# Kernel tuning notes

Hardware: AMD Instinct MI355X
Metric: run time of the kernel (lower is better)

The kernel has to match this reference:

```python
import jax, jax.numpy as jnp
import numpy as np

H = 256
B, S, N = 16, 64, 100


def setup_inputs() -> dict:
    key = jax.random.key(0)
    ks = jax.random.split(key, 12)
    def p(k, shape):
        return jax.random.normal(k, shape, dtype=jnp.float32) * 0.02
    z = lambda *s: jnp.zeros(s, jnp.float32)
    return {
        'x': jax.random.normal(ks[0], (B, S, N, H), dtype=jnp.float32),
        'W_ih0': p(ks[1], (4 * H, H)), 'W_hh0': p(ks[2], (4 * H, H)),
        'b_ih0': z(4 * H), 'b_hh0': z(4 * H),
        'W_ih1': p(ks[3], (4 * H, H)), 'W_hh1': p(ks[4], (4 * H, H)),
        'b_ih1': z(4 * H), 'b_hh1': z(4 * H),
        'ln_g': jnp.ones((H,), jnp.float32), 'ln_b': z(H),
        'cen_w1': p(ks[5], (H // 2, H)), 'cen_b1': z(H // 2),
        'cen_w2': p(ks[6], (4, H // 2)), 'cen_b2': z(4),
        'svd_w1': p(ks[7], (H // 2, H)), 'svd_b1': z(H // 2),
        'svd_w2': p(ks[8], (2, H // 2)), 'svd_b2': z(2),
        'lsvd_w1': p(ks[9], (H, H)), 'lsvd_b1': z(H),
        'lsvd_w2': p(ks[10], (16, H)), 'lsvd_b2': z(16),
        'steps': 10,
    }


def reference(x, W_ih0, W_hh0, b_ih0, b_hh0, W_ih1, W_hh1, b_ih1, b_hh1,
              ln_g, ln_b, cen_w1, cen_b1, cen_w2, cen_b2,
              svd_w1, svd_b1, svd_w2, svd_b2,
              lsvd_w1, lsvd_b1, lsvd_w2, lsvd_b2, steps):
    # Dropout layers are identity (eval mode). Per-node Python loop in the
    # original is vectorized by folding nodes into the batch dim (independent
    # LSTM chains share weights and zero-initialized hidden state).
    Bx, Sx, Nx, Hx = x.shape
    BN = Bx * Nx
    xb = x.transpose(0, 2, 1, 3).reshape(BN, Sx, Hx)  # [BN, S, H]

    def cell(xin, h, c, Wih, Whh, bih, bhh):
        g = xin @ Wih.T + bih + h @ Whh.T + bhh
        i, f, gg, o = jnp.split(g, 4, axis=-1)  # torch gate order i,f,g,o
        c = jax.nn.sigmoid(f) * c + jax.nn.sigmoid(i) * jnp.tanh(gg)
        h = jax.nn.sigmoid(o) * jnp.tanh(c)
        return h, c

    def ln(v):
        m = v.mean(-1, keepdims=True)
        var = ((v - m) ** 2).mean(-1, keepdims=True)
        return (v - m) / jnp.sqrt(var + 1e-5) * ln_g + ln_b

    def heads(h):
        cen = jnp.maximum(h @ cen_w1.T + cen_b1, 0.0) @ cen_w2.T + cen_b2
        svd = jnp.maximum(h @ svd_w1.T + svd_b1, 0.0) @ svd_w2.T + svd_b2
        lsvd = jnp.maximum(h @ lsvd_w1.T + lsvd_b1, 0.0) @ lsvd_w2.T + lsvd_b2
        return jnp.concatenate([cen, svd, lsvd], axis=-1)  # [BN, 22]

    zeros = jnp.zeros((BN, Hx), x.dtype)

    def enc_step(carry, xt):
        h0, c0, h1, c1 = carry
        h0, c0 = cell(xt, h0, c0, W_ih0, W_hh0, b_ih0, b_hh0)
        h1, c1 = cell(h0, h1, c1, W_ih1, W_hh1, b_ih1, b_hh1)
        return (h0, c0, h1, c1), None

    (h0, c0, h1, c1), _ = jax.lax.scan(enc_step, (zeros, zeros, zeros, zeros),
                                       xb.transpose(1, 0, 2))
    h_t = ln(h1)  # layernorm of last encoder output

    def dec_step(carry, _):
        ht, h0, c0, h1, c1 = carry
        pred = heads(ht)
        h0n, c0n = cell(ht, h0, c0, W_ih0, W_hh0, b_ih0, b_hh0)
        h1n, c1n = cell(h0n, h1, c1, W_ih1, W_hh1, b_ih1, b_hh1)
        return (ln(h1n), h0n, c0n, h1n, c1n), pred

    _, preds = jax.lax.scan(dec_step, (h_t, h0, c0, h1, c1), None, length=steps)
    # preds: [steps, BN, 22] -> [B, steps, N, 22]
    return preds.reshape(steps, Bx, Nx, 22).transpose(1, 0, 2, 3)
```

## Files before the change

### kernel.cpp

```cpp
#include <hip/hip_runtime.h>
#include <hip/hip_bf16.h>
#include <stdint.h>


#define H 256
#define SS 64
#define NN 100
#define BNROWS 1600
#define KD 512
#define STEPS 10

typedef __bf16 bf16_t;
typedef __attribute__((ext_vector_type(8))) __bf16 bf16x8;
typedef __attribute__((ext_vector_type(4))) __bf16 bf16x4;
typedef __attribute__((ext_vector_type(4))) float f32x4;
typedef __attribute__((ext_vector_type(4))) unsigned uint4v;

__device__ __forceinline__ float sigm(float x) { return 1.0f / (1.0f + __expf(-x)); }
__device__ __forceinline__ float tanh_c(float x) {
    x = fminf(fmaxf(x, -15.0f), 15.0f);
    float e = __expf(2.0f * x);
    return (e - 1.0f) / (e + 1.0f);
}

__device__ __forceinline__ unsigned ld_sys(const unsigned* p) {
    return __hip_atomic_load(p, __ATOMIC_RELAXED, __HIP_MEMORY_SCOPE_SYSTEM);
}
__device__ __forceinline__ void st_sys(unsigned* p, unsigned v) {
    __hip_atomic_store(p, v, __ATOMIC_RELAXED, __HIP_MEMORY_SCOPE_SYSTEM);
}
__device__ __forceinline__ uint4v ld16_sys(const void* p) {
    uint4v v;
    asm volatile("global_load_dwordx4 %0, %1, off sc0 sc1"
                 : "=v"(v) : "v"(p) : "memory");
    return v;
}
__device__ __forceinline__ unsigned pack_bf16(float a, float b) {
    bf16_t xa = (bf16_t)a, xb = (bf16_t)b;
    unsigned short ua, ub;
    __builtin_memcpy(&ua, &xa, 2);
    __builtin_memcpy(&ub, &xb, 2);
    return (unsigned)ua | ((unsigned)ub << 16);
}
__device__ __forceinline__ float bf16lo(unsigned u) {
    unsigned v = u << 16; float f; __builtin_memcpy(&f, &v, 4); return f;
}
__device__ __forceinline__ float bf16hi(unsigned u) {
    unsigned v = u & 0xffff0000u; float f; __builtin_memcpy(&f, &v, 4); return f;
}
__device__ __forceinline__ float u2f(unsigned u) {
    float f; __builtin_memcpy(&f, &u, 4); return f;
}
__device__ __forceinline__ unsigned f2u(float f) {
    unsigned u; __builtin_memcpy(&u, &f, 4); return u;
}

__global__ __launch_bounds__(256)
void prep_kernel(const float* __restrict__ Wih0, const float* __restrict__ Whh0,
                 const float* __restrict__ bih0, const float* __restrict__ bhh0,
                 const float* __restrict__ Wih1, const float* __restrict__ Whh1,
                 const float* __restrict__ bih1, const float* __restrict__ bhh1,
                 const float* __restrict__ cw1, const float* __restrict__ sw1,
                 const float* __restrict__ lw1,
                 const float* __restrict__ cb1, const float* __restrict__ sb1,
                 const float* __restrict__ lb1,
                 bf16_t* __restrict__ W0c, bf16_t* __restrict__ W1c,
                 bf16_t* __restrict__ Wh1, float* __restrict__ bias0,
                 float* __restrict__ bias1, float* __restrict__ biash)
{
    int idx = blockIdx.x * 256 + threadIdx.x;
    if (idx < 524288) {
        int nr = idx >> 9, k = idx & 511;
        int j = nr >> 2, gi = nr & 3;
        int go = gi * 256 + j;
        float v = (k < 256) ? Wih0[go * 256 + k] : Whh0[go * 256 + (k - 256)];
        W0c[idx] = (bf16_t)v;
        return;
    }
    idx -= 524288;
    if (idx < 524288) {
        int nr = idx >> 9, k = idx & 511;
        int j = nr >> 2, gi = nr & 3;
        int go = gi * 256 + j;
        float v = (k < 256) ? Wih1[go * 256 + k] : Whh1[go * 256 + (k - 256)];
        W1c[idx] = (bf16_t)v;
        return;
    }
    idx -= 524288;
    if (idx < 131072) {
        int r = idx >> 8, k = idx & 255;
        float v = (r < 128) ? cw1[r * 256 + k]
                            : (r < 256 ? sw1[(r - 128) * 256 + k]
                                       : lw1[(r - 256) * 256 + k]);
        Wh1[idx] = (bf16_t)v;
        return;
    }
    idx -= 131072;
    if (idx < 1024) {
        int j = idx >> 2, gi = idx & 3, go = gi * 256 + j;
        bias0[idx] = bih0[go] + bhh0[go];
        return;
    }
    idx -= 1024;
    if (idx < 1024) {
        int j = idx >> 2, gi = idx & 3, go = gi * 256 + j;
        bias1[idx] = bih1[go] + bhh1[go];
        return;
    }
    idx -= 1024;
    if (idx < 512) {
        biash[idx] = (idx < 128) ? cb1[idx]
                                 : (idx < 256 ? sb1[idx - 128] : lb1[idx - 256]);
    }
}

__global__ __launch_bounds__(256)
void xconv_kernel(const float* __restrict__ x, bf16_t* __restrict__ xb)
{
    int o = (blockIdx.x * 256 + threadIdx.x) * 4;
    int s = o / 409600;
    int rem = o - s * 409600;
    int m = rem >> 8;
    int h = rem & 255;
    int b = m / 100, n = m - b * 100;
    const float* src = x + (((size_t)(b * 64 + s) * 100 + n) << 8) + h;
    f32x4 v = *(const f32x4*)src;
    bf16x4 ov;
    ov[0] = (bf16_t)v.x; ov[1] = (bf16_t)v.y; ov[2] = (bf16_t)v.z; ov[3] = (bf16_t)v.w;
    *(bf16x4*)(xb + o) = ov;
}

struct PA {
    const bf16_t* xb;
    const bf16_t* W0c; const bf16_t* W1c; const bf16_t* Wh1;
    const float* bias0; const float* bias1; const float* biash;
    const float* lng; const float* lnb;
    const float* cw2; const float* cb2;
    const float* sw2; const float* sb2;
    const float* lw2; const float* lb2;
    bf16_t* h0a; bf16_t* h0b; bf16_t* h1a; bf16_t* h1b;
    bf16_t* ht; float* hid;
    unsigned* cnt;
    float* out;
};

__global__ __launch_bounds__(256, 2)
void persistent_kernel(PA p)
{
    __shared__ uint4v smem[4160];

    const int tid  = threadIdx.x;
    const int w    = tid >> 6;
    const int lane = tid & 63;
    const int quad = lane >> 4;
    const int l16  = lane & 15;
    const bool isL0 = (blockIdx.x < 200);
    const int cb   = isL0 ? (int)blockIdx.x : (int)blockIdx.x - 200;
    const int mt   = cb >> 3;
    const int nt   = cb & 7;
    const int bg   = nt + (isL0 ? 0 : 8);
    const int mbase = mt * 64;
    const int nbase = nt * 128 + w * 32;
    const int hcb   = nbase >> 2;
    float* Gw = (float*)smem + w * 2304;

    const int trow  = tid >> 6;
    const int tcol8 = (tid & 63) * 8;
    const bool firsthalf = (tcol8 < 256);
    const int coladj = firsthalf ? tcol8 : tcol8 - 256;
    const size_t stagebyte = ((size_t)(mbase + trow) * 256 + coladj) * 2;

    unsigned* cntg = p.cnt + mt * 64;
    unsigned rnd = 0;
    auto bar = [&]() {
        ++rnd;
        asm volatile("s_waitcnt vmcnt(0) lgkmcnt(0)" ::: "memory");
        __syncthreads();
        if (tid == 0) {
            __hip_atomic_fetch_add(cntg, 1u, __ATOMIC_RELAXED,
                                   __HIP_MEMORY_SCOPE_SYSTEM);
            while (__hip_atomic_load(cntg, __ATOMIC_RELAXED,
                                     __HIP_MEMORY_SCOPE_SYSTEM) < 16u * rnd) { }
        }
        __syncthreads();
    };

    bf16_t* h0buf[2] = { p.h0a, p.h0b };
    bf16_t* h1buf[2] = { p.h1a, p.h1b };

    float bv[2];
    {
        const float* br = isL0 ? p.bias0 : p.bias1;
        #pragma unroll
        for (int nf = 0; nf < 2; ++nf) bv[nf] = br[nbase + nf * 16 + l16];
    }
    const int hb1 = nt * 64 + w * 16;
    const float bh = p.biash[hb1 + l16];
    float lgv[4], lbv[4];
    #pragma unroll
    for (int j = 0; j < 4; ++j) { lgv[j] = p.lng[lane * 4 + j]; lbv[j] = p.lnb[lane * 4 + j]; }

    const bf16_t* Wc = isL0 ? p.W0c : p.W1c;
    bf16x8 Breg[2][16];
    #pragma unroll
    for (int nf = 0; nf < 2; ++nf)
        #pragma unroll
        for (int kf = 0; kf < 16; ++kf)
            Breg[nf][kf] = *(const bf16x8*)(Wc + (size_t)(nbase + nf * 16 + l16) * KD
                                            + kf * 32 + quad * 8);

    float creg[8];
    #pragma unroll
    for (int e = 0; e < 8; ++e) creg[e] = 0.0f;

    auto cellw = [&](const bf16_t* sA, const bf16_t* sB, bf16_t* hd) {
        {
            const char* sp = (const char*)(firsthalf ? sA : sB) + stagebyte;
            uint4v c[8];
            #pragma unroll
            for (int i = 0; i < 8; ++i) c[i] = ld16_sys(sp + (size_t)i * 2048);
            asm volatile("s_waitcnt vmcnt(0)" ::: "memory");
            #pragma unroll
            for (int i = 0; i < 8; ++i)
                *(uint4v*)((char*)smem + (size_t)(trow + i * 4) * 1040 + tcol8 * 2) = c[i];
            #pragma unroll
            for (int i = 0; i < 8; ++i) c[i] = ld16_sys(sp + (size_t)(i + 8) * 2048);
            asm volatile("s_waitcnt vmcnt(0)" ::: "memory");
            #pragma unroll
            for (int i = 0; i < 8; ++i)
                *(uint4v*)((char*)smem + (size_t)(trow + (i + 8) * 4) * 1040 + tcol8 * 2) = c[i];
        }
        __syncthreads();

        f32x4 zero4 = {0.f, 0.f, 0.f, 0.f};
        f32x4 acc[4][2];
        #pragma unroll
        for (int mf = 0; mf < 4; ++mf)
            #pragma unroll
            for (int nf = 0; nf < 2; ++nf) acc[mf][nf] = zero4;

        #pragma unroll
        for (int kf = 0; kf < 16; ++kf) {
            bf16x8 af[4];
            #pragma unroll
            for (int mf = 0; mf < 4; ++mf)
                af[mf] = *(const bf16x8*)((char*)smem
                            + (size_t)(mf * 16 + l16) * 1040 + kf * 64 + quad * 16);
            #pragma unroll
            for (int mf = 0; mf < 4; ++mf)
                #pragma unroll
                for (int nf = 0; nf < 2; ++nf)
                    acc[mf][nf] = __builtin_amdgcn_mfma_f32_16x16x32_bf16(
                        af[mf], Breg[nf][kf], acc[mf][nf], 0, 0, 0);
        }
        __syncthreads();

        #pragma unroll
        for (int mf = 0; mf < 4; ++mf)
            #pragma unroll
            for (int nf = 0; nf < 2; ++nf)
                #pragma unroll
                for (int r = 0; r < 4; ++r)
                    Gw[(mf * 16 + quad * 4 + r) * 36 + nf * 16 + l16] =
                        acc[mf][nf][r] + bv[nf];
        asm volatile("s_waitcnt lgkmcnt(0)" ::: "memory");

        #pragma unroll
        for (int e = 0; e < 4; ++e) {
            int ml  = e * 16 + (lane >> 2);
            int jl2 = (lane & 3) * 2;
            f32x4 ga = *(const f32x4*)(Gw + ml * 36 + jl2 * 4);
            f32x4 gb = *(const f32x4*)(Gw + ml * 36 + jl2 * 4 + 4);
            float cn0 = sigm(ga.y) * creg[e * 2] + sigm(ga.x) * tanh_c(ga.z);
            float cn1 = sigm(gb.y) * creg[e * 2 + 1] + sigm(gb.x) * tanh_c(gb.z);
            creg[e * 2]     = cn0;
            creg[e * 2 + 1] = cn1;
            float hn0 = sigm(ga.w) * tanh_c(cn0);
            float hn1 = sigm(gb.w) * tanh_c(cn1);
            st_sys((unsigned*)(hd + (size_t)(mbase + ml) * H + hcb + jl2),
                   pack_bf16(hn0, hn1));
        }
    };

    auto heads1w = [&]() {
        {
            const int hrow0 = tid >> 5;
            const int hcol8 = (tid & 31) * 8;
            const char* sp = (const char*)p.ht
                + ((size_t)(mbase + hrow0) * 256 + hcol8) * 2;
            uint4v c[8];
            #pragma unroll
            for (int i = 0; i < 8; ++i) c[i] = ld16_sys(sp + (size_t)i * 4096);
            asm volatile("s_waitcnt vmcnt(0)" ::: "memory");
            #pragma unroll
            for (int i = 0; i < 8; ++i)
                *(uint4v*)((char*)smem + (size_t)(hrow0 + i * 8) * 1040 + hcol8 * 2) = c[i];
        }
        __syncthreads();

        f32x4 zero4 = {0.f, 0.f, 0.f, 0.f};
        f32x4 ha[4] = {zero4, zero4, zero4, zero4};
        #pragma unroll
        for (int kf = 0; kf < 8; ++kf) {
            bf16x8 bb = *(const bf16x8*)(p.Wh1 + (size_t)(hb1 + l16) * H
                                         + kf * 32 + quad * 8);
            #pragma unroll
            for (int mf = 0; mf < 4; ++mf) {
                bf16x8 af = *(const bf16x8*)((char*)smem
                            + (size_t)(mf * 16 + l16) * 1040 + kf * 64 + quad * 16);
                ha[mf] = __builtin_amdgcn_mfma_f32_16x16x32_bf16(af, bb, ha[mf], 0, 0, 0);
            }
        }
        #pragma unroll
        for (int mf = 0; mf < 4; ++mf)
            #pragma unroll
            for (int r = 0; r < 4; ++r) {
                int mg = mbase + mf * 16 + quad * 4 + r;
                int ng = hb1 + l16;
                float v = fmaxf(ha[mf][r] + bh, 0.0f);
                st_sys((unsigned*)(p.hid + (size_t)mg * 512 + ng), f2u(v));
            }
    };

    auto heads2w = [&](int s) {
        int idx = nt * 256 + tid;
        if (idx >= 64 * 22) return;
        int lr = idx / 22;
        int o  = idx - lr * 22;
        int m  = mbase + lr;
        const unsigned* hrow = (const unsigned*)(p.hid + (size_t)m * 512);
        const float* wp; float bias; int k0, len;
        if (o < 4)      { wp = p.cw2 + o * 128;       bias = p.cb2[o];     k0 = 0;   len = 128; }
        else if (o < 6) { wp = p.sw2 + (o - 4) * 128; bias = p.sb2[o - 4]; k0 = 128; len = 128; }
        else            { wp = p.lw2 + (o - 6) * 256; bias = p.lb2[o - 6]; k0 = 256; len = 256; }
        float acc = bias;
        for (int k = 0; k < len; k += 4) {
            f32x4 wv = *(const f32x4*)(wp + k);
            acc += u2f(ld_sys(hrow + k0 + k))     * wv.x;
            acc += u2f(ld_sys(hrow + k0 + k + 1)) * wv.y;
            acc += u2f(ld_sys(hrow + k0 + k + 2)) * wv.z;
            acc += u2f(ld_sys(hrow + k0 + k + 3)) * wv.w;
        }
        int b = m / NN, n = m - b * NN;
        p.out[(((size_t)b * STEPS + s) * NN + n) * 22 + o] = acc;
    };

    auto lnw = [&](const bf16_t* src) {
        int sample = mbase + bg * 4 + w;
        const unsigned* rp = (const unsigned*)(src + (size_t)sample * H) + lane * 2;
        unsigned u0 = ld_sys(rp), u1 = ld_sys(rp + 1);
        float v[4] = { bf16lo(u0), bf16hi(u0), bf16lo(u1), bf16hi(u1) };
        float sm = v[0] + v[1] + v[2] + v[3];
        #pragma unroll
        for (int off = 32; off > 0; off >>= 1) sm += __shfl_xor(sm, off);
        float mean = sm * (1.0f / H);
        float q = 0.f;
        #pragma unroll
        for (int j = 0; j < 4; ++j) { float d = v[j] - mean; q += d * d; }
        #pragma unroll
        for (int off = 32; off > 0; off >>= 1) q += __shfl_xor(q, off);
        float rstd = rsqrtf(q * (1.0f / H) + 1e-5f);
        float o0 = (v[0] - mean) * rstd * lgv[0] + lbv[0];
        float o1 = (v[1] - mean) * rstd * lgv[1] + lbv[1];
        float o2 = (v[2] - mean) * rstd * lgv[2] + lbv[2];
        float o3 = (v[3] - mean) * rstd * lgv[3] + lbv[3];
        unsigned* wp2 = (unsigned*)(p.ht + (size_t)sample * H) + lane * 2;
        st_sys(wp2,     pack_bf16(o0, o1));
        st_sys(wp2 + 1, pack_bf16(o2, o3));
    };

    #pragma unroll 1
    for (int r = 0; r < 65; ++r) {
        if (isL0) {
            if (r < 64)
                cellw(p.xb + (size_t)r * 409600, h0buf[(r + 1) & 1], h0buf[r & 1]);
        } else {
            if (r >= 1)
                cellw(h0buf[(r + 1) & 1], h1buf[r & 1], h1buf[(r + 1) & 1]);
        }
        bar();
    }
    lnw(h1buf[1]);
    bar();

    #pragma unroll 1
    for (int s = 0; s < STEPS; ++s) {
        if (isL0) cellw(p.ht, h0buf[(s + 1) & 1], h0buf[s & 1]);
        else      heads1w();
        bar();
        if (!isL0) cellw(h0buf[s & 1], h1buf[(s + 1) & 1], h1buf[s & 1]);
        else       heads2w(s);
        bar();
        if (s < STEPS - 1) { lnw(h1buf[s & 1]); bar(); }
    }
}

__global__ __launch_bounds__(256)
void cell_kernel(const float* __restrict__ xsrc, int t,
                 const bf16_t* __restrict__ a1,
                 const bf16_t* __restrict__ a2,
                 const bf16_t* __restrict__ Wc,
                 const float* __restrict__ biasr,
                 float* __restrict__ cst,
                 bf16_t* __restrict__ hout)
{
    __shared__ char smem_raw[18432];
    bf16_t* As = (bf16_t*)smem_raw;
    bf16_t* Bs = (bf16_t*)(smem_raw + 9216);
    float*  Gsf = (float*)smem_raw;

    const int tid  = threadIdx.x;
    const int mblk = blockIdx.x;
    const int nblk = blockIdx.y;
    const int am = tid >> 2;
    const int kc = (tid & 3) << 4;
    const int gm = mblk * 64 + am;

    const float*  xrow  = nullptr;
    const bf16_t* arow1 = nullptr;
    if (xsrc) {
        int b = gm / NN;
        int n = gm - b * NN;
        xrow = xsrc + (((size_t)b * SS + t) * NN + n) * H;
    } else {
        arow1 = a1 + (size_t)gm * H;
    }
    const bf16_t* arow2 = a2 + (size_t)gm * H;
    const bf16_t* brow  = Wc + (size_t)(nblk * 64 + am) * KD;

    bf16x8 ra0, ra1, rb0, rb1;
    auto loadA = [&](int ko) {
        int k = ko + kc;
        if (xsrc) {
            if (k < 256) {
                const f32x4* pq = (const f32x4*)(xrow + k);
                f32x4 f0 = pq[0], f1 = pq[1], f2 = pq[2], f3 = pq[3];
                bf16x8 v0, v1;
                v0[0]=(bf16_t)f0.x; v0[1]=(bf16_t)f0.y; v0[2]=(bf16_t)f0.z; v0[3]=(bf16_t)f0.w;
                v0[4]=(bf16_t)f1.x; v0[5]=(bf16_t)f1.y; v0[6]=(bf16_t)f1.z; v0[7]=(bf16_t)f1.w;
                v1[0]=(bf16_t)f2.x; v1[1]=(bf16_t)f2.y; v1[2]=(bf16_t)f2.z; v1[3]=(bf16_t)f2.w;
                v1[4]=(bf16_t)f3.x; v1[5]=(bf16_t)f3.y; v1[6]=(bf16_t)f3.z; v1[7]=(bf16_t)f3.w;
                ra0 = v0; ra1 = v1;
            } else {
                const bf16x8* pq = (const bf16x8*)(arow2 + (k - 256));
                ra0 = pq[0]; ra1 = pq[1];
            }
        } else {
            const bf16x8* pq = (k < 256) ? (const bf16x8*)(arow1 + k)
                                         : (const bf16x8*)(arow2 + (k - 256));
            ra0 = pq[0]; ra1 = pq[1];
        }
    };
    auto loadB = [&](int ko) {
        const bf16x8* pq = (const bf16x8*)(brow + ko + kc);
        rb0 = pq[0]; rb1 = pq[1];
    };
    loadA(0); loadB(0);

    const int w    = tid >> 6;
    const int lane = tid & 63;
    const int wm   = w & 1, wn = w >> 1;
    const int quad = lane >> 4, l16 = lane & 15;

    f32x4 zero4 = {0.f, 0.f, 0.f, 0.f};
    f32x4 acc[2][2] = {{zero4, zero4}, {zero4, zero4}};

    for (int kk = 0; kk < 8; ++kk) {
        __syncthreads();
        *(bf16x8*)(As + am * 72 + kc)     = ra0;
        *(bf16x8*)(As + am * 72 + kc + 8) = ra1;
        *(bf16x8*)(Bs + am * 72 + kc)     = rb0;
        *(bf16x8*)(Bs + am * 72 + kc + 8) = rb1;
        __syncthreads();
        if (kk < 7) { loadA((kk + 1) * 64); loadB((kk + 1) * 64); }
        #pragma unroll
        for (int ks = 0; ks < 2; ++ks) {
            bf16x8 af[2], bb[2];
            #pragma unroll
            for (int mi = 0; mi < 2; ++mi)
                af[mi] = *(const bf16x8*)(As + (wm * 32 + mi * 16 + l16) * 72 + ks * 32 + quad * 8);
            #pragma unroll
            for (int ni = 0; ni < 2; ++ni)
                bb[ni] = *(const bf16x8*)(Bs + (wn * 32 + ni * 16 + l16) * 72 + ks * 32 + quad * 8);
            #pragma unroll
            for (int mi = 0; mi < 2; ++mi)
                #pragma unroll
                for (int ni = 0; ni < 2; ++ni)
                    acc[mi][ni] = __builtin_amdgcn_mfma_f32_16x16x32_bf16(
                        af[mi], bb[ni], acc[mi][ni], 0, 0, 0);
        }
    }

    __syncthreads();
    float bvv[2];
    #pragma unroll
    for (int ni = 0; ni < 2; ++ni)
        bvv[ni] = biasr[nblk * 64 + wn * 32 + ni * 16 + l16];

    #pragma unroll
    for (int mi = 0; mi < 2; ++mi)
        #pragma unroll
        for (int ni = 0; ni < 2; ++ni)
            #pragma unroll
            for (int r = 0; r < 4; ++r) {
                int ml = wm * 32 + mi * 16 + quad * 4 + r;
                int nl = wn * 32 + ni * 16 + l16;
                Gsf[ml * 68 + nl] = acc[mi][ni][r] + bvv[ni];
            }
    __syncthreads();

    #pragma unroll
    for (int e = 0; e < 4; ++e) {
        int id = tid + 256 * e;
        int ml = id >> 4;
        int jl = id & 15;
        f32x4 g4 = *(const f32x4*)(Gsf + ml * 68 + jl * 4);
        int gmm = mblk * 64 + ml;
        int jg  = nblk * 16 + jl;
        float co = cst[(size_t)gmm * H + jg];
        float iv = sigm(g4.x);
        float fv = sigm(g4.y);
        float gv = tanh_c(g4.z);
        float ov = sigm(g4.w);
        float cn = fv * co + iv * gv;
        float hn = ov * tanh_c(cn);
        cst[(size_t)gmm * H + jg]  = cn;
        hout[(size_t)gmm * H + jg] = (bf16_t)hn;
    }
}

__global__ __launch_bounds__(256)
void heads1_kernel(const bf16_t* __restrict__ a1,
                   const bf16_t* __restrict__ Wh,
                   const float* __restrict__ biash,
                   bf16_t* __restrict__ hid)
{
    __shared__ char smem_raw[18432];
    bf16_t* As = (bf16_t*)smem_raw;
    bf16_t* Bs = (bf16_t*)(smem_raw + 9216);

    const int tid  = threadIdx.x;
    const int mblk = blockIdx.x;
    const int nblk = blockIdx.y;
    const int am = tid >> 2;
    const int kc = (tid & 3) << 4;
    const int gm = mblk * 64 + am;
    const bf16_t* arow = a1 + (size_t)gm * H;
    const bf16_t* brow = Wh + (size_t)(nblk * 64 + am) * H;

    bf16x8 ra0, ra1, rb0, rb1;
    auto load = [&](int ko) {
        const bf16x8* pa = (const bf16x8*)(arow + ko + kc);
        ra0 = pa[0]; ra1 = pa[1];
        const bf16x8* pb = (const bf16x8*)(brow + ko + kc);
        rb0 = pb[0]; rb1 = pb[1];
    };
    load(0);

    const int w    = tid >> 6;
    const int lane = tid & 63;
    const int wm   = w & 1, wn = w >> 1;
    const int quad = lane >> 4, l16 = lane & 15;

    f32x4 zero4 = {0.f, 0.f, 0.f, 0.f};
    f32x4 acc[2][2] = {{zero4, zero4}, {zero4, zero4}};

    for (int kk = 0; kk < 4; ++kk) {
        __syncthreads();
        *(bf16x8*)(As + am * 72 + kc)     = ra0;
        *(bf16x8*)(As + am * 72 + kc + 8) = ra1;
        *(bf16x8*)(Bs + am * 72 + kc)     = rb0;
        *(bf16x8*)(Bs + am * 72 + kc + 8) = rb1;
        __syncthreads();
        if (kk < 3) load((kk + 1) * 64);
        #pragma unroll
        for (int ks = 0; ks < 2; ++ks) {
            bf16x8 af[2], bb[2];
            #pragma unroll
            for (int mi = 0; mi < 2; ++mi)
                af[mi] = *(const bf16x8*)(As + (wm * 32 + mi * 16 + l16) * 72 + ks * 32 + quad * 8);
            #pragma unroll
            for (int ni = 0; ni < 2; ++ni)
                bb[ni] = *(const bf16x8*)(Bs + (wn * 32 + ni * 16 + l16) * 72 + ks * 32 + quad * 8);
            #pragma unroll
            for (int mi = 0; mi < 2; ++mi)
                #pragma unroll
                for (int ni = 0; ni < 2; ++ni)
                    acc[mi][ni] = __builtin_amdgcn_mfma_f32_16x16x32_bf16(
                        af[mi], bb[ni], acc[mi][ni], 0, 0, 0);
        }
    }

    #pragma unroll
    for (int mi = 0; mi < 2; ++mi)
        #pragma unroll
        for (int ni = 0; ni < 2; ++ni)
            #pragma unroll
            for (int r = 0; r < 4; ++r) {
                int mg = mblk * 64 + wm * 32 + mi * 16 + quad * 4 + r;
                int ng = nblk * 64 + wn * 32 + ni * 16 + l16;
                float v = acc[mi][ni][r] + biash[ng];
                hid[(size_t)mg * 512 + ng] = (bf16_t)fmaxf(v, 0.0f);
            }
}

__global__ __launch_bounds__(256)
void heads2_kernel(const bf16_t* __restrict__ hid,
                   const float* __restrict__ cw2, const float* __restrict__ cb2,
                   const float* __restrict__ sw2, const float* __restrict__ sb2,
                   const float* __restrict__ lw2, const float* __restrict__ lb2,
                   float* __restrict__ out, int s)
{
    int idx = blockIdx.x * 256 + threadIdx.x;
    if (idx >= BNROWS * 22) return;
    int m = idx / 22;
    int o = idx - m * 22;
    const bf16_t* hrow = hid + (size_t)m * 512;
    const float* wp; float bias; int k0, len;
    if (o < 4)      { wp = cw2 + o * 128;       bias = cb2[o];     k0 = 0;   len = 128; }
    else if (o < 6) { wp = sw2 + (o - 4) * 128; bias = sb2[o - 4]; k0 = 128; len = 128; }
    else            { wp = lw2 + (o - 6) * 256; bias = lb2[o - 6]; k0 = 256; len = 256; }
    float acc = bias;
    for (int k = 0; k < len; k += 4) {
        f32x4 wv = *(const f32x4*)(wp + k);
        acc += (float)hrow[k0 + k]     * wv.x;
        acc += (float)hrow[k0 + k + 1] * wv.y;
        acc += (float)hrow[k0 + k + 2] * wv.z;
        acc += (float)hrow[k0 + k + 3] * wv.w;
    }
    int b = m / NN, n = m - b * NN;
    out[(((size_t)b * STEPS + s) * NN + n) * 22 + o] = acc;
}

__global__ __launch_bounds__(256)
void ln_kernel(const bf16_t* __restrict__ hin,
               const float* __restrict__ gam, const float* __restrict__ bet,
               bf16_t* __restrict__ hto)
{
    int w = threadIdx.x >> 6;
    int lane = threadIdx.x & 63;
    int sample = blockIdx.x * 4 + w;
    const bf16_t* row = hin + (size_t)sample * H;
    float v[4];
    #pragma unroll
    for (int j = 0; j < 4; ++j) v[j] = (float)row[lane * 4 + j];
    float sm = v[0] + v[1] + v[2] + v[3];
    #pragma unroll
    for (int off = 32; off > 0; off >>= 1) sm += __shfl_xor(sm, off);
    float mean = sm * (1.0f / H);
    float q = 0.f;
    #pragma unroll
    for (int j = 0; j < 4; ++j) { float d = v[j] - mean; q += d * d; }
    #pragma unroll
    for (int off = 32; off > 0; off >>= 1) q += __shfl_xor(q, off);
    float rstd = rsqrtf(q * (1.0f / H) + 1e-5f);
    #pragma unroll
    for (int j = 0; j < 4; ++j) {
        int idx = lane * 4 + j;
        float o = (v[j] - mean) * rstd * gam[idx] + bet[idx];
        hto[(size_t)sample * H + idx] = (bf16_t)o;
    }
}

extern "C" void kernel_launch(void* const* d_in, const int* in_sizes, int n_in,
                              void* d_out, int out_size, void* d_ws, size_t ws_size,
                              hipStream_t stream)
{
    const float* x    = (const float*)d_in[0];
    const float* Wih0 = (const float*)d_in[1];
    const float* Whh0 = (const float*)d_in[2];
    const float* bih0 = (const float*)d_in[3];
    const float* bhh0 = (const float*)d_in[4];
    const float* Wih1 = (const float*)d_in[5];
    const float* Whh1 = (const float*)d_in[6];
    const float* bih1 = (const float*)d_in[7];
    const float* bhh1 = (const float*)d_in[8];
    const float* lng  = (const float*)d_in[9];
    const float* lnb  = (const float*)d_in[10];
    const float* cw1  = (const float*)d_in[11];
    const float* cb1  = (const float*)d_in[12];
    const float* cw2  = (const float*)d_in[13];
    const float* cb2  = (const float*)d_in[14];
    const float* sw1  = (const float*)d_in[15];
    const float* sb1  = (const float*)d_in[16];
    const float* sw2  = (const float*)d_in[17];
    const float* sb2  = (const float*)d_in[18];
    const float* lw1  = (const float*)d_in[19];
    const float* lb1  = (const float*)d_in[20];
    const float* lw2  = (const float*)d_in[21];
    const float* lb2  = (const float*)d_in[22];
    float* out = (float*)d_out;

    char* ws = (char*)d_ws;
    if (ws_size < 62200000) return;

    bf16_t* W0c   = (bf16_t*)(ws);
    bf16_t* W1c   = (bf16_t*)(ws + 1048576);
    bf16_t* Wh1w  = (bf16_t*)(ws + 2097152);
    float*  bias0 = (float*)(ws + 2359296);
    float*  bias1 = (float*)(ws + 2363392);
    float*  biash = (float*)(ws + 2367488);
    char* st = ws + 2369536;
    bf16_t* h0a = (bf16_t*)st;
    bf16_t* h0b = (bf16_t*)(st + 819200);
    bf16_t* h1a = (bf16_t*)(st + 1638400);
    bf16_t* h1b = (bf16_t*)(st + 2457600);
    bf16_t* ht  = (bf16_t*)(st + 3276800);
    float*  hid = (float*)(st + 4096000);
    unsigned* cnt = (unsigned*)(st + 7372800);
    bf16_t* xb  = (bf16_t*)(st + 7379200);
    float* c0 = (float*)(st + 7379200);
    float* c1 = (float*)(st + 9017600);

    hipMemsetAsync(st, 0, 3276800, stream);
    hipMemsetAsync(cnt, 0, 6400, stream);

    prep_kernel<<<4615, 256, 0, stream>>>(Wih0, Whh0, bih0, bhh0,
                                          Wih1, Whh1, bih1, bhh1,
                                          cw1, sw1, lw1, cb1, sb1, lb1,
                                          W0c, W1c, Wh1w, bias0, bias1, biash);
    xconv_kernel<<<25600, 256, 0, stream>>>(x, xb);

    PA pa;
    pa.xb = xb; pa.W0c = W0c; pa.W1c = W1c; pa.Wh1 = Wh1w;
    pa.bias0 = bias0; pa.bias1 = bias1; pa.biash = biash;
    pa.lng = lng; pa.lnb = lnb;
    pa.cw2 = cw2; pa.cb2 = cb2; pa.sw2 = sw2; pa.sb2 = sb2;
    pa.lw2 = lw2; pa.lb2 = lb2;
    pa.h0a = h0a; pa.h0b = h0b; pa.h1a = h1a; pa.h1b = h1b;
    pa.ht = ht; pa.hid = hid; pa.cnt = cnt; pa.out = out;

    void* kargs[] = { &pa };
    hipError_t err = hipLaunchCooperativeKernel((void*)persistent_kernel,
                                                dim3(400), dim3(256),
                                                kargs, 0, stream);
    if (err == hipSuccess) return;

    hipMemsetAsync(c0, 0, 1638400, stream);
    hipMemsetAsync(c1, 0, 1638400, stream);
    bf16_t* hidb = (bf16_t*)hid;
    bf16_t* h0buf[2] = { h0a, h0b };
    bf16_t* h1buf[2] = { h1a, h1b };
    dim3 cg2(25, 16);
    int cur = 0;
    for (int t = 0; t < SS; ++t) {
        cell_kernel<<<cg2, 256, 0, stream>>>(x, t, nullptr, h0buf[cur], W0c, bias0,
                                             c0, h0buf[cur ^ 1]);
        cell_kernel<<<cg2, 256, 0, stream>>>(nullptr, 0, h0buf[cur ^ 1], h1buf[cur],
                                             W1c, bias1, c1, h1buf[cur ^ 1]);
        cur ^= 1;
    }
    ln_kernel<<<400, 256, 0, stream>>>(h1buf[cur], lng, lnb, ht);
    for (int s = 0; s < STEPS; ++s) {
        heads1_kernel<<<dim3(25, 8), 256, 0, stream>>>(ht, Wh1w, biash, hidb);
        heads2_kernel<<<138, 256, 0, stream>>>(hidb, cw2, cb2, sw2, sb2, lw2, lb2,
                                               out, s);
        cell_kernel<<<cg2, 256, 0, stream>>>(nullptr, 0, ht, h0buf[cur], W0c, bias0,
                                             c0, h0buf[cur ^ 1]);
        cell_kernel<<<cg2, 256, 0, stream>>>(nullptr, 0, h0buf[cur ^ 1], h1buf[cur],
                                             W1c, bias1, c1, h1buf[cur ^ 1]);
        cur ^= 1;
        ln_kernel<<<400, 256, 0, stream>>>(h1buf[cur], lng, lnb, ht);
    }
}
```

Before: 1.257 ms.

## Use per-block flag barrier, transposed MFMA cell epilogue, and bf16 head hidden

Replaces the atomic-counter group barrier with per-block flag stores that are polled using vector loads, which removes contended atomics. The MFMA operands are swapped so each lane holds all four gates of a hidden unit in registers. The LSTM cell update then runs directly from the accumulators, skipping the fp32 LDS gate round-trip and one __syncthreads. Outputs go through a small LDS transpose into coalesced 16-byte system-scope stores. The heads hidden buffer changes from fp32 to bf16 and is read with vector loads, which cuts traffic but adds rounding error to the heads.

```diff
diff --git a/kernel.cpp b/kernel.cpp
--- a/kernel.cpp
+++ b/kernel.cpp
@@ -22,19 +22,6 @@
     float e = __expf(2.0f * x);
     return (e - 1.0f) / (e + 1.0f);
 }
-
-__device__ __forceinline__ unsigned ld_sys(const unsigned* p) {
-    return __hip_atomic_load(p, __ATOMIC_RELAXED, __HIP_MEMORY_SCOPE_SYSTEM);
-}
-__device__ __forceinline__ void st_sys(unsigned* p, unsigned v) {
-    __hip_atomic_store(p, v, __ATOMIC_RELAXED, __HIP_MEMORY_SCOPE_SYSTEM);
-}
-__device__ __forceinline__ uint4v ld16_sys(const void* p) {
-    uint4v v;
-    asm volatile("global_load_dwordx4 %0, %1, off sc0 sc1"
-                 : "=v"(v) : "v"(p) : "memory");
-    return v;
-}
 __device__ __forceinline__ unsigned pack_bf16(float a, float b) {
     bf16_t xa = (bf16_t)a, xb = (bf16_t)b;
     unsigned short ua, ub;
@@ -48,12 +35,22 @@
 __device__ __forceinline__ float bf16hi(unsigned u) {
     unsigned v = u & 0xffff0000u; float f; __builtin_memcpy(&f, &v, 4); return f;
 }
-__device__ __forceinline__ float u2f(unsigned u) {
-    float f; __builtin_memcpy(&f, &u, 4); return f;
-}
-__device__ __forceinline__ unsigned f2u(float f) {
-    unsigned u; __builtin_memcpy(&u, &f, 4); return u;
-}
+__device__ __forceinline__ uint4v ld16_sys(const void* p) {
+    uint4v v;
+    asm volatile("global_load_dwordx4 %0, %1, off sc0 sc1"
+                 : "=v"(v) : "v"(p) : "memory");
+    return v;
+}
+__device__ __forceinline__ void st16_sys(void* p, uint4v v) {
+    asm volatile("global_store_dwordx4 %0, %1, off sc0 sc1" :: "v"(p), "v"(v) : "memory");
+}
+__device__ __forceinline__ void st4_sys(void* p, unsigned v) {
+    asm volatile("global_store_dword %0, %1, off sc0 sc1" :: "v"(p), "v"(v) : "memory");
+}
+__device__ __forceinline__ unsigned ld4_sys(const unsigned* p) {
+    return __hip_atomic_load(p, __ATOMIC_RELAXED, __HIP_MEMORY_SCOPE_SYSTEM);
+}
+#define VM_DRAIN() asm volatile("s_waitcnt vmcnt(0)" ::: "memory")
 
 __global__ __launch_bounds__(256)
 void prep_kernel(const float* __restrict__ Wih0, const float* __restrict__ Whh0,
@@ -139,15 +136,16 @@
     const float* sw2; const float* sb2;
     const float* lw2; const float* lb2;
     bf16_t* h0a; bf16_t* h0b; bf16_t* h1a; bf16_t* h1b;
-    bf16_t* ht; float* hid;
-    unsigned* cnt;
+    bf16_t* ht; bf16_t* hid;
+    unsigned* flags;
     float* out;
 };
 
 __global__ __launch_bounds__(256, 2)
 void persistent_kernel(PA p)
 {
-    __shared__ uint4v smem[4160];
+    __shared__ char stageLDS[66560];
+    __shared__ char tbuf[8192];
 
     const int tid  = threadIdx.x;
     const int w    = tid >> 6;
@@ -156,31 +154,33 @@
     const int l16  = lane & 15;
     const bool isL0 = (blockIdx.x < 200);
     const int cb   = isL0 ? (int)blockIdx.x : (int)blockIdx.x - 200;
-    const int mt   = cb >> 3;
+    const int grp  = cb >> 3;
     const int nt   = cb & 7;
     const int bg   = nt + (isL0 ? 0 : 8);
-    const int mbase = mt * 64;
+    const int mbase = grp * 64;
     const int nbase = nt * 128 + w * 32;
-    const int hcb   = nbase >> 2;
-    float* Gw = (float*)smem + w * 2304;
-
-    const int trow  = tid >> 6;
-    const int tcol8 = (tid & 63) * 8;
-    const bool firsthalf = (tcol8 < 256);
-    const int coladj = firsthalf ? tcol8 : tcol8 - 256;
-    const size_t stagebyte = ((size_t)(mbase + trow) * 256 + coladj) * 2;
-
-    unsigned* cntg = p.cnt + mt * 64;
+    const int hb    = nt * 64 + w * 16;
+
+    unsigned* fl = p.flags + grp * 64;
     unsigned rnd = 0;
     auto bar = [&]() {
         ++rnd;
-        asm volatile("s_waitcnt vmcnt(0) lgkmcnt(0)" ::: "memory");
+        VM_DRAIN();
         __syncthreads();
         if (tid == 0) {
-            __hip_atomic_fetch_add(cntg, 1u, __ATOMIC_RELAXED,
-                                   __HIP_MEMORY_SCOPE_SYSTEM);
-            while (__hip_atomic_load(cntg, __ATOMIC_RELAXED,
-                                     __HIP_MEMORY_SCOPE_SYSTEM) < 16u * rnd) { }
+            st4_sys(fl + bg, rnd);
+            for (;;) {
+                uint4v a = ld16_sys(fl);
+                uint4v b = ld16_sys(fl + 4);
+                uint4v c = ld16_sys(fl + 8);
+                uint4v d = ld16_sys(fl + 12);
+                VM_DRAIN();
+                unsigned m = min(min(min(a[0], a[1]), min(a[2], a[3])),
+                                 min(min(b[0], b[1]), min(b[2], b[3])));
+                m = min(m, min(min(min(c[0], c[1]), min(c[2], c[3])),
+                               min(min(d[0], d[1]), min(d[2], d[3]))));
+                if (m >= rnd) break;
+            }
         }
         __syncthreads();
     };
@@ -188,138 +188,122 @@
     bf16_t* h0buf[2] = { p.h0a, p.h0b };
     bf16_t* h1buf[2] = { p.h1a, p.h1b };
 
-    float bv[2];
-    {
-        const float* br = isL0 ? p.bias0 : p.bias1;
-        #pragma unroll
-        for (int nf = 0; nf < 2; ++nf) bv[nf] = br[nbase + nf * 16 + l16];
-    }
-    const int hb1 = nt * 64 + w * 16;
-    const float bh = p.biash[hb1 + l16];
-    float lgv[4], lbv[4];
-    #pragma unroll
-    for (int j = 0; j < 4; ++j) { lgv[j] = p.lng[lane * 4 + j]; lbv[j] = p.lnb[lane * 4 + j]; }
-
     const bf16_t* Wc = isL0 ? p.W0c : p.W1c;
     bf16x8 Breg[2][16];
     #pragma unroll
-    for (int nf = 0; nf < 2; ++nf)
+    for (int gt = 0; gt < 2; ++gt)
         #pragma unroll
         for (int kf = 0; kf < 16; ++kf)
-            Breg[nf][kf] = *(const bf16x8*)(Wc + (size_t)(nbase + nf * 16 + l16) * KD
+            Breg[gt][kf] = *(const bf16x8*)(Wc + (size_t)(nbase + gt * 16 + l16) * KD
                                             + kf * 32 + quad * 8);
+    const float* br = isL0 ? p.bias0 : p.bias1;
+    f32x4 bvq[2];
+    bvq[0] = *(const f32x4*)(br + nbase + quad * 4);
+    bvq[1] = *(const f32x4*)(br + nbase + 16 + quad * 4);
+    f32x4 bhq = *(const f32x4*)(p.biash + hb + quad * 4);
+    float lgv[4], lbv[4];
+    #pragma unroll
+    for (int j = 0; j < 4; ++j) { lgv[j] = p.lng[lane * 4 + j]; lbv[j] = p.lnb[lane * 4 + j]; }
 
     float creg[8];
     #pragma unroll
     for (int e = 0; e < 8; ++e) creg[e] = 0.0f;
 
-    auto cellw = [&](const bf16_t* sA, const bf16_t* sB, bf16_t* hd) {
-        {
-            const char* sp = (const char*)(firsthalf ? sA : sB) + stagebyte;
-            uint4v c[8];
-            #pragma unroll
-            for (int i = 0; i < 8; ++i) c[i] = ld16_sys(sp + (size_t)i * 2048);
-            asm volatile("s_waitcnt vmcnt(0)" ::: "memory");
-            #pragma unroll
-            for (int i = 0; i < 8; ++i)
-                *(uint4v*)((char*)smem + (size_t)(trow + i * 4) * 1040 + tcol8 * 2) = c[i];
-            #pragma unroll
-            for (int i = 0; i < 8; ++i) c[i] = ld16_sys(sp + (size_t)(i + 8) * 2048);
-            asm volatile("s_waitcnt vmcnt(0)" ::: "memory");
-            #pragma unroll
-            for (int i = 0; i < 8; ++i)
-                *(uint4v*)((char*)smem + (size_t)(trow + (i + 8) * 4) * 1040 + tcol8 * 2) = c[i];
-        }
+    auto stage2 = [&](const bf16_t* s1, const bf16_t* s2) {
+        const char* sel = (lane < 32) ? (const char*)s1 : ((const char*)s2 - 512);
+        const char* gp = sel + (size_t)(mbase + w * 16) * 512 + lane * 16;
+        uint4v t[16];
+        #pragma unroll
+        for (int i = 0; i < 16; ++i) t[i] = ld16_sys(gp + (size_t)i * 512);
+        VM_DRAIN();
+        char* lp = stageLDS + (w * 16) * 1040 + lane * 16;
+        #pragma unroll
+        for (int i = 0; i < 16; ++i) *(uint4v*)(lp + i * 1040) = t[i];
         __syncthreads();
-
+    };
+
+    auto cellw = [&](const bf16_t* s1, const bf16_t* s2, bf16_t* hd) {
+        stage2(s1, s2);
         f32x4 zero4 = {0.f, 0.f, 0.f, 0.f};
-        f32x4 acc[4][2];
-        #pragma unroll
-        for (int mf = 0; mf < 4; ++mf)
-            #pragma unroll
-            for (int nf = 0; nf < 2; ++nf) acc[mf][nf] = zero4;
-
+        f32x4 acc[2][4];
+        #pragma unroll
+        for (int gt = 0; gt < 2; ++gt)
+            #pragma unroll
+            for (int mt = 0; mt < 4; ++mt) acc[gt][mt] = zero4;
         #pragma unroll
         for (int kf = 0; kf < 16; ++kf) {
             bf16x8 af[4];
             #pragma unroll
-            for (int mf = 0; mf < 4; ++mf)
-                af[mf] = *(const bf16x8*)((char*)smem
-                            + (size_t)(mf * 16 + l16) * 1040 + kf * 64 + quad * 16);
-            #pragma unroll
-            for (int mf = 0; mf < 4; ++mf)
+            for (int mt = 0; mt < 4; ++mt)
+                af[mt] = *(const bf16x8*)(stageLDS + (size_t)(mt * 16 + l16) * 1040
+                                          + kf * 64 + quad * 16);
+            #pragma unroll
+            for (int gt = 0; gt < 2; ++gt)
                 #pragma unroll
-                for (int nf = 0; nf < 2; ++nf)
-                    acc[mf][nf] = __builtin_amdgcn_mfma_f32_16x16x32_bf16(
-                        af[mf], Breg[nf][kf], acc[mf][nf], 0, 0, 0);
-        }
-        __syncthreads();
-
-        #pragma unroll
-        for (int mf = 0; mf < 4; ++mf)
-            #pragma unroll
-            for (int nf = 0; nf < 2; ++nf)
-                #pragma unroll
-                for (int r = 0; r < 4; ++r)
-                    Gw[(mf * 16 + quad * 4 + r) * 36 + nf * 16 + l16] =
-                        acc[mf][nf][r] + bv[nf];
+                for (int mt = 0; mt < 4; ++mt)
+                    acc[gt][mt] = __builtin_amdgcn_mfma_f32_16x16x32_bf16(
+                        Breg[gt][kf], af[mt], acc[gt][mt], 0, 0, 0);
+        }
+        bf16_t* tb = (bf16_t*)(tbuf + w * 2048);
+        #pragma unroll
+        for (int gt = 0; gt < 2; ++gt)
+            #pragma unroll
+            for (int mt = 0; mt < 4; ++mt) {
+                f32x4 g4 = acc[gt][mt] + bvq[gt];
+                int ci = gt * 4 + mt;
+                float cn = sigm(g4.y) * creg[ci] + sigm(g4.x) * tanh_c(g4.z);
+                creg[ci] = cn;
+                tb[(mt * 16 + l16) * 8 + gt * 4 + quad] = (bf16_t)(sigm(g4.w) * tanh_c(cn));
+            }
         asm volatile("s_waitcnt lgkmcnt(0)" ::: "memory");
-
-        #pragma unroll
-        for (int e = 0; e < 4; ++e) {
-            int ml  = e * 16 + (lane >> 2);
-            int jl2 = (lane & 3) * 2;
-            f32x4 ga = *(const f32x4*)(Gw + ml * 36 + jl2 * 4);
-            f32x4 gb = *(const f32x4*)(Gw + ml * 36 + jl2 * 4 + 4);
-            float cn0 = sigm(ga.y) * creg[e * 2] + sigm(ga.x) * tanh_c(ga.z);
-            float cn1 = sigm(gb.y) * creg[e * 2 + 1] + sigm(gb.x) * tanh_c(gb.z);
-            creg[e * 2]     = cn0;
-            creg[e * 2 + 1] = cn1;
-            float hn0 = sigm(ga.w) * tanh_c(cn0);
-            float hn1 = sigm(gb.w) * tanh_c(cn1);
-            st_sys((unsigned*)(hd + (size_t)(mbase + ml) * H + hcb + jl2),
-                   pack_bf16(hn0, hn1));
-        }
+        bf16x8 hv = *(const bf16x8*)(tb + lane * 8);
+        st16_sys((char*)hd + ((size_t)(mbase + lane) * 256 + nt * 32 + w * 8) * 2,
+                 *(uint4v*)&hv);
     };
 
     auto heads1w = [&]() {
         {
             const int hrow0 = tid >> 5;
             const int hcol8 = (tid & 31) * 8;
-            const char* sp = (const char*)p.ht
+            const char* gp = (const char*)p.ht
                 + ((size_t)(mbase + hrow0) * 256 + hcol8) * 2;
-            uint4v c[8];
-            #pragma unroll
-            for (int i = 0; i < 8; ++i) c[i] = ld16_sys(sp + (size_t)i * 4096);
-            asm volatile("s_waitcnt vmcnt(0)" ::: "memory");
+            uint4v t[8];
+            #pragma unroll
+            for (int i = 0; i < 8; ++i) t[i] = ld16_sys(gp + (size_t)i * 4096);
+            VM_DRAIN();
             #pragma unroll
             for (int i = 0; i < 8; ++i)
-                *(uint4v*)((char*)smem + (size_t)(hrow0 + i * 8) * 1040 + hcol8 * 2) = c[i];
+                *(uint4v*)(stageLDS + (size_t)(hrow0 + i * 8) * 1040 + hcol8 * 2) = t[i];
         }
         __syncthreads();
-
         f32x4 zero4 = {0.f, 0.f, 0.f, 0.f};
         f32x4 ha[4] = {zero4, zero4, zero4, zero4};
         #pragma unroll
         for (int kf = 0; kf < 8; ++kf) {
-            bf16x8 bb = *(const bf16x8*)(p.Wh1 + (size_t)(hb1 + l16) * H
+            bf16x8 bb = *(const bf16x8*)(p.Wh1 + (size_t)(hb + l16) * 256
                                          + kf * 32 + quad * 8);
             #pragma unroll
-            for (int mf = 0; mf < 4; ++mf) {
-                bf16x8 af = *(const bf16x8*)((char*)smem
-                            + (size_t)(mf * 16 + l16) * 1040 + kf * 64 + quad * 16);
-                ha[mf] = __builtin_amdgcn_mfma_f32_16x16x32_bf16(af, bb, ha[mf], 0, 0, 0);
+            for (int mt = 0; mt < 4; ++mt) {
+                bf16x8 af = *(const bf16x8*)(stageLDS + (size_t)(mt * 16 + l16) * 1040
+                                             + kf * 64 + quad * 16);
+                ha[mt] = __builtin_amdgcn_mfma_f32_16x16x32_bf16(bb, af, ha[mt], 0, 0, 0);
             }
         }
-        #pragma unroll
-        for (int mf = 0; mf < 4; ++mf)
-            #pragma unroll
-            for (int r = 0; r < 4; ++r) {
-                int mg = mbase + mf * 16 + quad * 4 + r;
-                int ng = hb1 + l16;
-                float v = fmaxf(ha[mf][r] + bh, 0.0f);
-                st_sys((unsigned*)(p.hid + (size_t)mg * 512 + ng), f2u(v));
-            }
+        bf16_t* tb = (bf16_t*)(tbuf + w * 2048);
+        #pragma unroll
+        for (int mt = 0; mt < 4; ++mt) {
+            f32x4 v = ha[mt] + bhq;
+            bf16x4 pk;
+            #pragma unroll
+            for (int r = 0; r < 4; ++r) pk[r] = (bf16_t)fmaxf(v[r], 0.0f);
+            *(bf16x4*)(tb + (mt * 16 + l16) * 16 + quad * 4) = pk;
+        }
+        asm volatile("s_waitcnt lgkmcnt(0)" ::: "memory");
+        bf16x8 v0 = *(const bf16x8*)(tb + lane * 16);
+        bf16x8 v1 = *(const bf16x8*)(tb + lane * 16 + 8);
+        char* dst = (char*)p.hid + ((size_t)(mbase + lane) * 512 + hb) * 2;
+        st16_sys(dst, *(uint4v*)&v0);
+        st16_sys(dst + 16, *(uint4v*)&v1);
     };
 
     auto heads2w = [&](int s) {
@@ -328,18 +312,29 @@
         int lr = idx / 22;
         int o  = idx - lr * 22;
         int m  = mbase + lr;
-        const unsigned* hrow = (const unsigned*)(p.hid + (size_t)m * 512);
+        const char* hrow = (const char*)(p.hid + (size_t)m * 512);
         const float* wp; float bias; int k0, len;
         if (o < 4)      { wp = p.cw2 + o * 128;       bias = p.cb2[o];     k0 = 0;   len = 128; }
         else if (o < 6) { wp = p.sw2 + (o - 4) * 128; bias = p.sb2[o - 4]; k0 = 128; len = 128; }
         else            { wp = p.lw2 + (o - 6) * 256; bias = p.lb2[o - 6]; k0 = 256; len = 256; }
         float acc = bias;
-        for (int k = 0; k < len; k += 4) {
-            f32x4 wv = *(const f32x4*)(wp + k);
-            acc += u2f(ld_sys(hrow + k0 + k))     * wv.x;
-            acc += u2f(ld_sys(hrow + k0 + k + 1)) * wv.y;
-            acc += u2f(ld_sys(hrow + k0 + k + 2)) * wv.z;
-            acc += u2f(ld_sys(hrow + k0 + k + 3)) * wv.w;
+        for (int kb = 0; kb < len; kb += 64) {
+            uint4v hv[8];
+            #pragma unroll
+            for (int i = 0; i < 8; ++i)
+                hv[i] = ld16_sys(hrow + (size_t)(k0 + kb + i * 8) * 2);
+            VM_DRAIN();
+            #pragma unroll
+            for (int i = 0; i < 8; ++i) {
+                bf16x8 h8 = *(bf16x8*)&hv[i];
+                const float* wpp = wp + kb + i * 8;
+                f32x4 w0 = *(const f32x4*)wpp;
+                f32x4 w1 = *(const f32x4*)(wpp + 4);
+                acc += (float)h8[0] * w0.x + (float)h8[1] * w0.y
+                     + (float)h8[2] * w0.z + (float)h8[3] * w0.w
+                     + (float)h8[4] * w1.x + (float)h8[5] * w1.y
+                     + (float)h8[6] * w1.z + (float)h8[7] * w1.w;
+            }
         }
         int b = m / NN, n = m - b * NN;
         p.out[(((size_t)b * STEPS + s) * NN + n) * 22 + o] = acc;
@@ -348,7 +343,7 @@
     auto lnw = [&](const bf16_t* src) {
         int sample = mbase + bg * 4 + w;
         const unsigned* rp = (const unsigned*)(src + (size_t)sample * H) + lane * 2;
-        unsigned u0 = ld_sys(rp), u1 = ld_sys(rp + 1);
+        unsigned u0 = ld4_sys(rp), u1 = ld4_sys(rp + 1);
         float v[4] = { bf16lo(u0), bf16hi(u0), bf16lo(u1), bf16hi(u1) };
         float sm = v[0] + v[1] + v[2] + v[3];
         #pragma unroll
@@ -365,8 +360,8 @@
         float o2 = (v[2] - mean) * rstd * lgv[2] + lbv[2];
         float o3 = (v[3] - mean) * rstd * lgv[3] + lbv[3];
         unsigned* wp2 = (unsigned*)(p.ht + (size_t)sample * H) + lane * 2;
-        st_sys(wp2,     pack_bf16(o0, o1));
-        st_sys(wp2 + 1, pack_bf16(o2, o3));
+        st4_sys(wp2,     pack_bf16(o0, o1));
+        st4_sys(wp2 + 1, pack_bf16(o2, o3));
     };
 
     #pragma unroll 1
@@ -434,12 +429,12 @@
         if (xsrc) {
             if (k < 256) {
                 const f32x4* pq = (const f32x4*)(xrow + k);
-                f32x4 f0 = pq[0], f1 = pq[1], f2 = pq[2], f3 = pq[3];
+                f32x4 fq0 = pq[0], fq1 = pq[1], fq2 = pq[2], fq3 = pq[3];
                 bf16x8 v0, v1;
-                v0[0]=(bf16_t)f0.x; v0[1]=(bf16_t)f0.y; v0[2]=(bf16_t)f0.z; v0[3]=(bf16_t)f0.w;
-                v0[4]=(bf16_t)f1.x; v0[5]=(bf16_t)f1.y; v0[6]=(bf16_t)f1.z; v0[7]=(bf16_t)f1.w;
-                v1[0]=(bf16_t)f2.x; v1[1]=(bf16_t)f2.y; v1[2]=(bf16_t)f2.z; v1[3]=(bf16_t)f2.w;
-                v1[4]=(bf16_t)f3.x; v1[5]=(bf16_t)f3.y; v1[6]=(bf16_t)f3.z; v1[7]=(bf16_t)f3.w;
+                v0[0]=(bf16_t)fq0.x; v0[1]=(bf16_t)fq0.y; v0[2]=(bf16_t)fq0.z; v0[3]=(bf16_t)fq0.w;
+                v0[4]=(bf16_t)fq1.x; v0[5]=(bf16_t)fq1.y; v0[6]=(bf16_t)fq1.z; v0[7]=(bf16_t)fq1.w;
+                v1[0]=(bf16_t)fq2.x; v1[1]=(bf16_t)fq2.y; v1[2]=(bf16_t)fq2.z; v1[3]=(bf16_t)fq2.w;
+                v1[4]=(bf16_t)fq3.x; v1[5]=(bf16_t)fq3.y; v1[6]=(bf16_t)fq3.z; v1[7]=(bf16_t)fq3.w;
                 ra0 = v0; ra1 = v1;
             } else {
                 const bf16x8* pq = (const bf16x8*)(arow2 + (k - 256));
@@ -518,14 +513,9 @@
         int gmm = mblk * 64 + ml;
         int jg  = nblk * 16 + jl;
         float co = cst[(size_t)gmm * H + jg];
-        float iv = sigm(g4.x);
-        float fv = sigm(g4.y);
-        float gv = tanh_c(g4.z);
-        float ov = sigm(g4.w);
-        float cn = fv * co + iv * gv;
-        float hn = ov * tanh_c(cn);
+        float cn = sigm(g4.y) * co + sigm(g4.x) * tanh_c(g4.z);
         cst[(size_t)gmm * H + jg]  = cn;
-        hout[(size_t)gmm * H + jg] = (bf16_t)hn;
+        hout[(size_t)gmm * H + jg] = (bf16_t)(sigm(g4.w) * tanh_c(cn));
     }
 }
 
@@ -692,7 +682,7 @@
     float* out = (float*)d_out;
 
     char* ws = (char*)d_ws;
-    if (ws_size < 62200000) return;
+    if (ws_size < 65000000) return;
 
     bf16_t* W0c   = (bf16_t*)(ws);
     bf16_t* W1c   = (bf16_t*)(ws + 1048576);
@@ -706,16 +696,16 @@
     bf16_t* h1a = (bf16_t*)(st + 1638400);
     bf16_t* h1b = (bf16_t*)(st + 2457600);
     bf16_t* ht  = (bf16_t*)(st + 3276800);
-    float*  hid = (float*)(st + 4096000);
-    unsigned* cnt = (unsigned*)(st + 7372800);
-    bf16_t* xb  = (bf16_t*)(st + 7379200);
-    float* c0 = (float*)(st + 7379200);
-    float* c1 = (float*)(st + 9017600);
+    bf16_t* hid = (bf16_t*)(st + 4096000);
+    unsigned* flg = (unsigned*)(st + 5734400);
+    bf16_t* xb  = (bf16_t*)(st + 5740800);
+    float* fc0 = (float*)(st + 5740800);
+    float* fc1 = (float*)(st + 7379200);
 
     hipMemsetAsync(st, 0, 3276800, stream);
-    hipMemsetAsync(cnt, 0, 6400, stream);
-
-    prep_kernel<<<4615, 256, 0, stream>>>(Wih0, Whh0, bih0, bhh0,
+    hipMemsetAsync(flg, 0, 6400, stream);
+
+    prep_kernel<<<4618, 256, 0, stream>>>(Wih0, Whh0, bih0, bhh0,
                                           Wih1, Whh1, bih1, bhh1,
                                           cw1, sw1, lw1, cb1, sb1, lb1,
                                           W0c, W1c, Wh1w, bias0, bias1, biash);
@@ -728,7 +718,7 @@
     pa.cw2 = cw2; pa.cb2 = cb2; pa.sw2 = sw2; pa.sb2 = sb2;
     pa.lw2 = lw2; pa.lb2 = lb2;
     pa.h0a = h0a; pa.h0b = h0b; pa.h1a = h1a; pa.h1b = h1b;
-    pa.ht = ht; pa.hid = hid; pa.cnt = cnt; pa.out = out;
+    pa.ht = ht; pa.hid = hid; pa.flags = flg; pa.out = out;
 
     void* kargs[] = { &pa };
     hipError_t err = hipLaunchCooperativeKernel((void*)persistent_kernel,
@@ -736,29 +726,28 @@
                                                 kargs, 0, stream);
     if (err == hipSuccess) return;
 
-    hipMemsetAsync(c0, 0, 1638400, stream);
-    hipMemsetAsync(c1, 0, 1638400, stream);
-    bf16_t* hidb = (bf16_t*)hid;
+    hipMemsetAsync(fc0, 0, 1638400, stream);
+    hipMemsetAsync(fc1, 0, 1638400, stream);
     bf16_t* h0buf[2] = { h0a, h0b };
     bf16_t* h1buf[2] = { h1a, h1b };
     dim3 cg2(25, 16);
     int cur = 0;
     for (int t = 0; t < SS; ++t) {
         cell_kernel<<<cg2, 256, 0, stream>>>(x, t, nullptr, h0buf[cur], W0c, bias0,
-                                             c0, h0buf[cur ^ 1]);
+                                             fc0, h0buf[cur ^ 1]);
         cell_kernel<<<cg2, 256, 0, stream>>>(nullptr, 0, h0buf[cur ^ 1], h1buf[cur],
-                                             W1c, bias1, c1, h1buf[cur ^ 1]);
+                                             W1c, bias1, fc1, h1buf[cur ^ 1]);
         cur ^= 1;
     }
     ln_kernel<<<400, 256, 0, stream>>>(h1buf[cur], lng, lnb, ht);
     for (int s = 0; s < STEPS; ++s) {
-        heads1_kernel<<<dim3(25, 8), 256, 0, stream>>>(ht, Wh1w, biash, hidb);
-        heads2_kernel<<<138, 256, 0, stream>>>(hidb, cw2, cb2, sw2, sb2, lw2, lb2,
+        heads1_kernel<<<dim3(25, 8), 256, 0, stream>>>(ht, Wh1w, biash, hid);
+        heads2_kernel<<<138, 256, 0, stream>>>(hid, cw2, cb2, sw2, sb2, lw2, lb2,
                                                out, s);
         cell_kernel<<<cg2, 256, 0, stream>>>(nullptr, 0, ht, h0buf[cur], W0c, bias0,
-                                             c0, h0buf[cur ^ 1]);
+                                             fc0, h0buf[cur ^ 1]);
         cell_kernel<<<cg2, 256, 0, stream>>>(nullptr, 0, h0buf[cur ^ 1], h1buf[cur],
-                                             W1c, bias1, c1, h1buf[cur ^ 1]);
+                                             W1c, bias1, fc1, h1buf[cur ^ 1]);
         cur ^= 1;
         ln_kernel<<<400, 256, 0, stream>>>(h1buf[cur], lng, lnb, ht);
     }
```

Measured after the change: 1.101 ms. 1.14x faster.
